# Kernel tuning notes

Hardware: AMD Instinct MI355X
Metric: run time of the kernel (lower is better)

## Reference

```python
import jax, jax.numpy as jnp
import numpy as np

QUERY_DIM, FEAT_DIM, HID_DIM, OUT_DIM = 512, 2048, 512, 512
B, L, S, T = 8, 128, 100, 100


def setup_inputs() -> dict:
    key = jax.random.key(0)
    ks = jax.random.split(key, 9)
    d = {
        "query": jax.random.normal(ks[0], (B, L, QUERY_DIM), jnp.float32),
        "src": jax.random.normal(ks[1], (B, S, FEAT_DIM), jnp.float32),
        "trg": jax.random.normal(ks[2], (B, T, FEAT_DIM), jnp.float32),
        # params (LinearAct == Linear + identity act); src/trg projections share weights
        "Wq": jax.random.normal(ks[3], (QUERY_DIM, HID_DIM), jnp.float32) / np.sqrt(QUERY_DIM),
        "bq": jnp.zeros((HID_DIM,), jnp.float32),
        "Ws": jax.random.normal(ks[4], (FEAT_DIM, HID_DIM), jnp.float32) / np.sqrt(FEAT_DIM),
        "bs": jnp.zeros((HID_DIM,), jnp.float32),
        "Wo": jax.random.normal(ks[5], (HID_DIM + QUERY_DIM, OUT_DIM), jnp.float32) / np.sqrt(HID_DIM + QUERY_DIM),
        "bo": jnp.zeros((OUT_DIM,), jnp.float32),
    }
    return d


def reference(query, src, trg, Wq, bq, Ws, bs, Wo, bo):
    b, l, _ = query.shape
    s = src.shape[1]
    t = trg.shape[1]
    q = query @ Wq + bq          # b,l,k
    s_key = src @ Ws + bs        # b,s,k
    t_key = trg @ Ws + bs        # b,t,k
    hid = q.shape[-1]
    # score[b,l,s,t] = q . (s_key - t_key)/sqrt(2) / sqrt(hid) -- decomposed, no b,s,t,k tensor
    qs = jnp.einsum('blk,bsk->bls', q, s_key)
    qt = jnp.einsum('blk,btk->blt', q, t_key)
    score = (qs[:, :, :, None] - qt[:, :, None, :]) / jnp.sqrt(jnp.asarray(2.0 * hid, q.dtype))
    w = jax.nn.softmax(score.reshape(b, l, s * t), axis=-1).reshape(b, l, s, t)
    # ctx = sum_{s,t} w * (s_key - t_key)/sqrt(2), decomposed via marginals
    ws = w.sum(axis=3)           # b,l,s
    wt = w.sum(axis=2)           # b,l,t
    ctx = (jnp.einsum('bls,bsk->blk', ws, s_key) - jnp.einsum('blt,btk->blk', wt, t_key)) / jnp.sqrt(jnp.asarray(2.0, q.dtype))
    x = jnp.concatenate([query, ctx], axis=-1) @ Wo + bo
    return x
```

## Files before the change

### kernel.cpp

```cpp
#include <hip/hip_runtime.h>
#include <math.h>


typedef __attribute__((ext_vector_type(8))) short s16x8;
typedef __attribute__((ext_vector_type(4))) float f32x4;

__device__ __forceinline__ unsigned short f2bf(float f) {
    unsigned int u = __float_as_uint(f);
    return (unsigned short)((u + 0x7fffu + ((u >> 16) & 1u)) >> 16);
}

__device__ __forceinline__ s16x8 cvt8(const float* p) {
    float4 u = *(const float4*)p, w = *(const float4*)(p + 4);
    s16x8 o;
    o[0] = (short)f2bf(u.x); o[1] = (short)f2bf(u.y);
    o[2] = (short)f2bf(u.z); o[3] = (short)f2bf(u.w);
    o[4] = (short)f2bf(w.x); o[5] = (short)f2bf(w.y);
    o[6] = (short)f2bf(w.z); o[7] = (short)f2bf(w.w);
    return o;
}

__device__ __forceinline__ void gemm64_keys(
    const float* __restrict__ src, const float* __restrict__ trg,
    const float* __restrict__ Ws, unsigned short* __restrict__ Kb,
    int m0, int n0, unsigned short* As, unsigned short* Bs) {
    const int t = threadIdx.x;
    const int lane = t & 63, wid = t >> 6;
    const int wm = (wid & 1) * 32, wn = (wid >> 1) * 32;
    const int lr = lane & 15, lq = lane >> 4;
    const int r = t >> 3, c8 = (t & 7) * 8;
    const int nrow = t >> 2, kc16 = (t & 3) * 16;

    const int ra_row = m0 + r, rb_row = m0 + r + 32;
    const float* arp = (ra_row < 800) ? (src + (size_t)ra_row * 2048)
                                      : (trg + (size_t)(ra_row - 800) * 2048);
    const float* brp = (rb_row < 800) ? (src + (size_t)rb_row * 2048)
                                      : (trg + (size_t)(rb_row - 800) * 2048);

    s16x8 ra0, ra1;
    float bw[16];
#define LDK(kt)                                                              \
    ra0 = cvt8(arp + (kt) + c8);                                             \
    ra1 = cvt8(brp + (kt) + c8);                                             \
    _Pragma("unroll")                                                        \
    for (int j = 0; j < 16; j++)                                             \
        bw[j] = Ws[(size_t)((kt) + kc16 + j) * 512 + n0 + nrow];

    f32x4 acc[2][2] = {};
    LDK(0);
    for (int it = 0; it < 32; it++) {
        __syncthreads();
        *(s16x8*)&As[r * 72 + c8]        = ra0;
        *(s16x8*)&As[(r + 32) * 72 + c8] = ra1;
        {
            s16x8 bb0, bb1;
#pragma unroll
            for (int j = 0; j < 8; j++) {
                bb0[j] = (short)f2bf(bw[j]);
                bb1[j] = (short)f2bf(bw[8 + j]);
            }
            *(s16x8*)&Bs[nrow * 72 + kc16]     = bb0;
            *(s16x8*)&Bs[nrow * 72 + kc16 + 8] = bb1;
        }
        __syncthreads();
        if (it < 31) { LDK((it + 1) * 64); }
#pragma unroll
        for (int s = 0; s < 2; s++) {
            s16x8 a0 = *(const s16x8*)&As[(wm + lr) * 72      + s * 32 + lq * 8];
            s16x8 a1 = *(const s16x8*)&As[(wm + 16 + lr) * 72 + s * 32 + lq * 8];
            s16x8 b0 = *(const s16x8*)&Bs[(wn + lr) * 72      + s * 32 + lq * 8];
            s16x8 b1 = *(const s16x8*)&Bs[(wn + 16 + lr) * 72 + s * 32 + lq * 8];
            acc[0][0] = __builtin_amdgcn_mfma_f32_16x16x32_bf16(a0, b0, acc[0][0], 0, 0, 0);
            acc[0][1] = __builtin_amdgcn_mfma_f32_16x16x32_bf16(a0, b1, acc[0][1], 0, 0, 0);
            acc[1][0] = __builtin_amdgcn_mfma_f32_16x16x32_bf16(a1, b0, acc[1][0], 0, 0, 0);
            acc[1][1] = __builtin_amdgcn_mfma_f32_16x16x32_bf16(a1, b1, acc[1][1], 0, 0, 0);
        }
    }
#undef LDK
#pragma unroll
    for (int i = 0; i < 2; i++)
#pragma unroll
        for (int j = 0; j < 2; j++) {
            const int col = n0 + wn + j * 16 + lr;
            const int row = m0 + wm + i * 16 + lq * 4;
#pragma unroll
            for (int rr = 0; rr < 4; rr++)
                Kb[(size_t)(row + rr) * 512 + col] = f2bf(acc[i][j][rr]);
        }
}

__device__ __forceinline__ void gemm32_rawB(
    const float* __restrict__ A, const float* __restrict__ W,
    const float* __restrict__ bias, unsigned short* __restrict__ C,
    int m0, int n0, unsigned short* As, unsigned short* Bs) {
    const int t = threadIdx.x;
    const int lane = t & 63, wid = t >> 6;
    const int wm = (wid & 1) * 16, wn = (wid >> 1) * 32;
    const int lr = lane & 15, lq = lane >> 4;
    const int r = t >> 3, c8 = (t & 7) * 8;
    const int nrow = t >> 2, kc16 = (t & 3) * 16;

    s16x8 ra;
    float bw[16];
#define LDQ(kt)                                                              \
    ra = cvt8(A + (size_t)(m0 + r) * 512 + (kt) + c8);                       \
    _Pragma("unroll")                                                        \
    for (int j = 0; j < 16; j++)                                             \
        bw[j] = W[(size_t)((kt) + kc16 + j) * 512 + n0 + nrow];

    f32x4 acc[2] = {};
    LDQ(0);
    for (int it = 0; it < 8; it++) {
        __syncthreads();
        *(s16x8*)&As[r * 72 + c8] = ra;
        {
            s16x8 bb0, bb1;
#pragma unroll
            for (int j = 0; j < 8; j++) {
                bb0[j] = (short)f2bf(bw[j]);
                bb1[j] = (short)f2bf(bw[8 + j]);
            }
            *(s16x8*)&Bs[nrow * 72 + kc16]     = bb0;
            *(s16x8*)&Bs[nrow * 72 + kc16 + 8] = bb1;
        }
        __syncthreads();
        if (it < 7) { LDQ((it + 1) * 64); }
#pragma unroll
        for (int s = 0; s < 2; s++) {
            s16x8 a0 = *(const s16x8*)&As[(wm + lr) * 72      + s * 32 + lq * 8];
            s16x8 b0 = *(const s16x8*)&Bs[(wn + lr) * 72      + s * 32 + lq * 8];
            s16x8 b1 = *(const s16x8*)&Bs[(wn + 16 + lr) * 72 + s * 32 + lq * 8];
            acc[0] = __builtin_amdgcn_mfma_f32_16x16x32_bf16(a0, b0, acc[0], 0, 0, 0);
            acc[1] = __builtin_amdgcn_mfma_f32_16x16x32_bf16(a0, b1, acc[1], 0, 0, 0);
        }
    }
#undef LDQ
#pragma unroll
    for (int j = 0; j < 2; j++) {
        const int col = n0 + wn + j * 16 + lr;
        const int row = m0 + wm + lq * 4;
        const float bv = bias[col];
#pragma unroll
        for (int rr = 0; rr < 4; rr++)
            C[(size_t)(row + rr) * 512 + col] = f2bf(acc[j][rr] + bv);
    }
}

__device__ __forceinline__ void gemm32_cvtA(
    const float* __restrict__ A, const unsigned short* __restrict__ BT,
    const float* __restrict__ bias, float* __restrict__ C,
    int m0, int n0, int KB, unsigned short* As, unsigned short* Bs) {
    const int t = threadIdx.x;
    const int lane = t & 63, wid = t >> 6;
    const int wm = (wid & 1) * 16, wn = (wid >> 1) * 32;
    const int lr = lane & 15, lq = lane >> 4;
    const int r = t >> 3, c8 = (t & 7) * 8;

    s16x8 ra, rb0, rb1;
#define LD32(kt)                                                            \
    ra  = cvt8(A + (size_t)(m0 + r) * 512 + (kt) + c8);                     \
    rb0 = *(const s16x8*)(BT + (size_t)(n0 + r)      * KB + (kt) + c8);     \
    rb1 = *(const s16x8*)(BT + (size_t)(n0 + r + 32) * KB + (kt) + c8);

    f32x4 acc[2] = {};
    LD32(0);
    for (int it = 0; it < 8; it++) {
        __syncthreads();
        *(s16x8*)&As[r * 72 + c8]        = ra;
        *(s16x8*)&Bs[r * 72 + c8]        = rb0;
        *(s16x8*)&Bs[(r + 32) * 72 + c8] = rb1;
        __syncthreads();
        if (it < 7) { LD32((it + 1) * 64); }
#pragma unroll
        for (int s = 0; s < 2; s++) {
            s16x8 a0 = *(const s16x8*)&As[(wm + lr) * 72      + s * 32 + lq * 8];
            s16x8 b0 = *(const s16x8*)&Bs[(wn + lr) * 72      + s * 32 + lq * 8];
            s16x8 b1 = *(const s16x8*)&Bs[(wn + 16 + lr) * 72 + s * 32 + lq * 8];
            acc[0] = __builtin_amdgcn_mfma_f32_16x16x32_bf16(a0, b0, acc[0], 0, 0, 0);
            acc[1] = __builtin_amdgcn_mfma_f32_16x16x32_bf16(a0, b1, acc[1], 0, 0, 0);
        }
    }
#undef LD32
#pragma unroll
    for (int j = 0; j < 2; j++) {
        const int col = n0 + wn + j * 16 + lr;
        const int row = m0 + wm + lq * 4;
        const float bv = bias[col];
#pragma unroll
        for (int rr = 0; rr < 4; rr++)
            C[(size_t)(row + rr) * 512 + col] = acc[j][rr] + bv;
    }
}

__device__ __forceinline__ void gemm64_P(
    const unsigned short* __restrict__ Kb, const unsigned short* __restrict__ wotBot,
    float* __restrict__ P, int m0, int n0, unsigned short* As,
    unsigned short* Bs) {
    const int t = threadIdx.x;
    const int lane = t & 63, wid = t >> 6;
    const int wm = (wid & 1) * 32, wn = (wid >> 1) * 32;
    const int lr = lane & 15, lq = lane >> 4;
    const int r = t >> 3, c8 = (t & 7) * 8;

    s16x8 ra0, ra1, rb0, rb1;
#define LDP(kt)                                                               \
    ra0 = *(const s16x8*)(Kb + (size_t)(m0 + r)      * 512 + (kt) + c8);      \
    ra1 = *(const s16x8*)(Kb + (size_t)(m0 + r + 32) * 512 + (kt) + c8);      \
    rb0 = *(const s16x8*)(wotBot + (size_t)(n0 + r)      * 1024 + (kt) + c8); \
    rb1 = *(const s16x8*)(wotBot + (size_t)(n0 + r + 32) * 1024 + (kt) + c8);

    f32x4 acc[2][2] = {};
    LDP(0);
    for (int it = 0; it < 8; it++) {
        __syncthreads();
        *(s16x8*)&As[r * 72 + c8]        = ra0;
        *(s16x8*)&As[(r + 32) * 72 + c8] = ra1;
        *(s16x8*)&Bs[r * 72 + c8]        = rb0;
        *(s16x8*)&Bs[(r + 32) * 72 + c8] = rb1;
        __syncthreads();
        if (it < 7) { LDP((it + 1) * 64); }
#pragma unroll
        for (int s = 0; s < 2; s++) {
            s16x8 a0 = *(const s16x8*)&As[(wm + lr) * 72      + s * 32 + lq * 8];
            s16x8 a1 = *(const s16x8*)&As[(wm + 16 + lr) * 72 + s * 32 + lq * 8];
            s16x8 b0 = *(const s16x8*)&Bs[(wn + lr) * 72      + s * 32 + lq * 8];
            s16x8 b1 = *(const s16x8*)&Bs[(wn + 16 + lr) * 72 + s * 32 + lq * 8];
            acc[0][0] = __builtin_amdgcn_mfma_f32_16x16x32_bf16(a0, b0, acc[0][0], 0, 0, 0);
            acc[0][1] = __builtin_amdgcn_mfma_f32_16x16x32_bf16(a0, b1, acc[0][1], 0, 0, 0);
            acc[1][0] = __builtin_amdgcn_mfma_f32_16x16x32_bf16(a1, b0, acc[1][0], 0, 0, 0);
            acc[1][1] = __builtin_amdgcn_mfma_f32_16x16x32_bf16(a1, b1, acc[1][1], 0, 0, 0);
        }
    }
#undef LDP
#pragma unroll
    for (int i = 0; i < 2; i++)
#pragma unroll
        for (int j = 0; j < 2; j++) {
            const int col = n0 + wn + j * 16 + lr;
            const int row = m0 + wm + i * 16 + lq * 4;
#pragma unroll
            for (int rr = 0; rr < 4; rr++)
                P[(size_t)(row + rr) * 512 + col] = acc[i][j][rr];
        }
}

__global__ __launch_bounds__(256) void k_stage1(
    const float* __restrict__ query, const float* __restrict__ src,
    const float* __restrict__ trg, const float* __restrict__ Wq,
    const float* __restrict__ Ws, const float* __restrict__ Wo,
    const float* __restrict__ bq, unsigned short* __restrict__ qh,
    unsigned short* __restrict__ keysbf, unsigned short* __restrict__ wot) {
    __shared__ __align__(16) unsigned short As[64 * 72];
    __shared__ __align__(16) unsigned short Bs[64 * 72];
    const int bid = blockIdx.x, t = threadIdx.x;

    if (bid < 200) {
        gemm64_keys(src, trg, Ws, keysbf, (bid >> 3) * 64, (bid & 7) * 64,
                    As, Bs);
    } else if (bid < 456) {
        const int rr = bid - 200;
        gemm32_rawB(query, Wq, bq, qh, (rr >> 3) * 32, (rr & 7) * 64, As, Bs);
    } else {
        float (*tile)[33] = (float(*)[33])As;
        const int id2 = bid - 456;
        const int tk = id2 >> 4, tn = id2 & 15;
        const int row = t >> 3, c4 = (t & 7) * 4;
        float4 v = *(const float4*)(Wo + (size_t)(tk * 32 + row) * 512 + tn * 32 + c4);
        tile[row][c4 + 0] = v.x; tile[row][c4 + 1] = v.y;
        tile[row][c4 + 2] = v.z; tile[row][c4 + 3] = v.w;
        __syncthreads();
        ushort4 o = make_ushort4(f2bf(tile[c4 + 0][row]), f2bf(tile[c4 + 1][row]),
                                 f2bf(tile[c4 + 2][row]), f2bf(tile[c4 + 3][row]));
        *(ushort4*)(wot + (size_t)(tn * 32 + row) * 1024 + tk * 32 + c4) = o;
    }
}

__global__ __launch_bounds__(256) void k_stage2(
    const float* __restrict__ query, const unsigned short* __restrict__ qh,
    const unsigned short* __restrict__ keysbf,
    const unsigned short* __restrict__ wot, const float* __restrict__ bo,
    float* __restrict__ sc, float* __restrict__ P, float* __restrict__ out) {
    __shared__ __align__(16) unsigned short As[64 * 72];
    __shared__ __align__(16) unsigned short Bs[64 * 72];
    const int bid = blockIdx.x;
    const int t = threadIdx.x;

    if (bid >= 328) {
        const int rr = bid - 328;
        gemm32_cvtA(query, wot, bo, out, (rr >> 3) * 32, (rr & 7) * 64, 1024,
                    As, Bs);
        return;
    }
    if (bid >= 128) {
        const int rem = bid - 128;
        gemm64_P(keysbf, wot + 512, P, (rem >> 3) * 64, (rem & 7) * 64, As, Bs);
        return;
    }

    const int mt = bid >> 2, nt = bid & 3;
    const int m0 = mt * 32, b = mt >> 2, n0 = nt * 64;
    const int lane = t & 63, wid = t >> 6;
    const int wm = (wid & 1) * 16, wn = (wid >> 1) * 32;
    const int lr = lane & 15, lq = lane >> 4;
    const int r = t >> 3, c8 = (t & 7) * 8;

    const int nA = n0 + r, nB = n0 + r + 32;
    int kr0 = (nA < 128) ? (b * 100 + nA) : (800 + b * 100 + (nA - 128));
    int kr1 = (nB < 128) ? (b * 100 + nB) : (800 + b * 100 + (nB - 128));
    kr0 = kr0 > 1599 ? 1599 : kr0;
    kr1 = kr1 > 1599 ? 1599 : kr1;

    s16x8 ra, rb0, rb1;
#define LDSC(kt)                                                        \
    ra  = *(const s16x8*)(qh + (size_t)(m0 + r) * 512 + (kt) + c8);     \
    rb0 = *(const s16x8*)(keysbf + (size_t)kr0 * 512 + (kt) + c8);      \
    rb1 = *(const s16x8*)(keysbf + (size_t)kr1 * 512 + (kt) + c8);

    f32x4 acc[2] = {};
    LDSC(0);
    for (int it = 0; it < 8; it++) {
        __syncthreads();
        *(s16x8*)&As[r * 72 + c8]        = ra;
        *(s16x8*)&Bs[r * 72 + c8]        = rb0;
        *(s16x8*)&Bs[(r + 32) * 72 + c8] = rb1;
        __syncthreads();
        if (it < 7) { LDSC((it + 1) * 64); }
#pragma unroll
        for (int s = 0; s < 2; s++) {
            s16x8 a0 = *(const s16x8*)&As[(wm + lr) * 72      + s * 32 + lq * 8];
            s16x8 b0 = *(const s16x8*)&Bs[(wn + lr) * 72      + s * 32 + lq * 8];
            s16x8 b1 = *(const s16x8*)&Bs[(wn + 16 + lr) * 72 + s * 32 + lq * 8];
            acc[0] = __builtin_amdgcn_mfma_f32_16x16x32_bf16(a0, b0, acc[0], 0, 0, 0);
            acc[1] = __builtin_amdgcn_mfma_f32_16x16x32_bf16(a0, b1, acc[1], 0, 0, 0);
        }
    }
#undef LDSC
#pragma unroll
    for (int j = 0; j < 2; j++) {
        const int col = n0 + wn + j * 16 + lr;
        const int row = m0 + wm + lq * 4;
        const float scale = (col >= 128) ? -(1.0f / 32.0f) : (1.0f / 32.0f);
#pragma unroll
        for (int rr = 0; rr < 4; rr++)
            sc[(size_t)(row + rr) * 256 + col] = acc[j][rr] * scale;
    }
}

__global__ __launch_bounds__(256) void k_stageD(
    const float* __restrict__ sc, const float* __restrict__ P,
    float* __restrict__ out) {
    __shared__ float wbuf[200 * 33];
    __shared__ float Bs[40 * 32];

    const int t = threadIdx.x;
    const int b = blockIdx.y;
    const int n0 = blockIdx.x * 32;
    const int l0 = blockIdx.z * 32;
    const int wave = t >> 6, lane = t & 63;

    for (int i = 0; i < 8; i++) {
        const int li = wave * 8 + i;
        const float4 v = *(const float4*)(
            sc + (size_t)(b * 128 + l0 + li) * 256 + lane * 4);
        const float vv[4] = {v.x, v.y, v.z, v.w};
        const int c0 = lane * 4;
        float mS = -1e30f, mT = -1e30f;
#pragma unroll
        for (int j = 0; j < 4; j++) {
            const int col = c0 + j;
            if (col < 100) mS = fmaxf(mS, vv[j]);
            if (col >= 128 && col < 228) mT = fmaxf(mT, vv[j]);
        }
#pragma unroll
        for (int off = 32; off > 0; off >>= 1) {
            mS = fmaxf(mS, __shfl_xor(mS, off));
            mT = fmaxf(mT, __shfl_xor(mT, off));
        }
        float eS[4], eT[4], sS = 0.f, sT = 0.f;
#pragma unroll
        for (int j = 0; j < 4; j++) {
            const int col = c0 + j;
            eS[j] = (col < 100) ? __expf(vv[j] - mS) : 0.f;
            eT[j] = (col >= 128 && col < 228) ? __expf(vv[j] - mT) : 0.f;
            sS += eS[j]; sT += eT[j];
        }
#pragma unroll
        for (int off = 32; off > 0; off >>= 1) {
            sS += __shfl_xor(sS, off);
            sT += __shfl_xor(sT, off);
        }
        const float iS = 1.f / sS, iT = 1.f / sT;
#pragma unroll
        for (int j = 0; j < 4; j++) {
            const int col = c0 + j;
            if (col < 100) wbuf[col * 33 + li] = eS[j] * iS;
            if (col >= 128 && col < 228)
                wbuf[(100 + col - 128) * 33 + li] = eT[j] * iT;
        }
    }
    __syncthreads();

    const int tx = t & 7, ty = t >> 3;
    float rB[5];
    auto loadB = [&](int kbase) {
#pragma unroll
        for (int e = 0; e < 5; e++) {
            const int idx = t + e * 256;
            const int k = idx >> 5, j = idx & 31;
            const int kk = kbase + k;
            rB[e] = (kk < 100)
                ?  P[(size_t)(b * 100 + kk) * 512 + n0 + j]
                : -P[(size_t)(800 + b * 100 + (kk - 100)) * 512 + n0 + j];
        }
    };

    float acc[4] = {};
    loadB(0);
    for (int c5 = 0; c5 < 5; c5++) {
        __syncthreads();
#pragma unroll
        for (int e = 0; e < 5; e++) {
            const int idx = t + e * 256;
            Bs[idx] = rB[e];
        }
        __syncthreads();
        if (c5 < 4) loadB((c5 + 1) * 40);
#pragma unroll 8
        for (int k = 0; k < 40; k++) {
            const float ar = wbuf[(c5 * 40 + k) * 33 + ty];
            float br[4];
            *(float4*)br = *(const float4*)&Bs[k * 32 + tx * 4];
#pragma unroll
            for (int j = 0; j < 4; j++) acc[j] = fmaf(ar, br[j], acc[j]);
        }
    }

    const float s2 = 0.70710678118654752f;
    const int m = b * 128 + l0 + ty;
#pragma unroll
    for (int j = 0; j < 4; j++)
        unsafeAtomicAdd(&out[(size_t)m * 512 + n0 + tx * 4 + j], acc[j] * s2);
}


extern "C" void kernel_launch(void* const* d_in, const int* in_sizes, int n_in,
                              void* d_out, int out_size, void* d_ws, size_t ws_size,
                              hipStream_t stream) {
    const float* query = (const float*)d_in[0];
    const float* src   = (const float*)d_in[1];
    const float* trg   = (const float*)d_in[2];
    const float* Wq    = (const float*)d_in[3];
    const float* bq    = (const float*)d_in[4];
    const float* Ws    = (const float*)d_in[5];
    const float* Wo    = (const float*)d_in[7];
    const float* bo    = (const float*)d_in[8];
    float* out = (float*)d_out;

    unsigned short* keysbf = (unsigned short*)d_ws;
    float* sc = (float*)(keysbf + 819200);
    float* P  = sc + 262144;
    unsigned short* qh  = (unsigned short*)(P + 819200);
    unsigned short* wot = qh + 524288;

    k_stage1<<<968, 256, 0, stream>>>(query, src, trg, Wq, Ws, Wo, bq,
                                      qh, keysbf, wot);
    k_stage2<<<584, 256, 0, stream>>>(query, qh, keysbf, wot, bo, sc, P, out);
    k_stageD<<<dim3(16, 8, 4), 256, 0, stream>>>(sc, P, out);
}
```

Baseline: 153.4 us.

## Split-K the key projection GEMM four ways with atomic fp32 accumulation

The src/trg key projection (1600x2048 by 2048x512) is split along K into four chunks of 512, giving 800 blocks instead of 200. Partial sums are accumulated with atomic adds into an fp32 keys buffer that is zeroed by a memset beforehand. Downstream consumers now read fp32 keys and convert them to bf16 on load. This is meant to fill the GPU better during stage 1, at the cost of an extra memset, atomic traffic, and doubled key read bandwidth in stage 2.

```diff
diff --git a/kernel.cpp b/kernel.cpp
--- a/kernel.cpp
+++ b/kernel.cpp
@@ -22,8 +22,8 @@
 
 __device__ __forceinline__ void gemm64_keys(
     const float* __restrict__ src, const float* __restrict__ trg,
-    const float* __restrict__ Ws, unsigned short* __restrict__ Kb,
-    int m0, int n0, unsigned short* As, unsigned short* Bs) {
+    const float* __restrict__ Ws, float* __restrict__ Kf,
+    int m0, int n0, int kbase, unsigned short* As, unsigned short* Bs) {
     const int t = threadIdx.x;
     const int lane = t & 63, wid = t >> 6;
     const int wm = (wid & 1) * 32, wn = (wid >> 1) * 32;
@@ -47,8 +47,8 @@
         bw[j] = Ws[(size_t)((kt) + kc16 + j) * 512 + n0 + nrow];
 
     f32x4 acc[2][2] = {};
-    LDK(0);
-    for (int it = 0; it < 32; it++) {
+    LDK(kbase);
+    for (int it = 0; it < 8; it++) {
         __syncthreads();
         *(s16x8*)&As[r * 72 + c8]        = ra0;
         *(s16x8*)&As[(r + 32) * 72 + c8] = ra1;
@@ -63,7 +63,7 @@
             *(s16x8*)&Bs[nrow * 72 + kc16 + 8] = bb1;
         }
         __syncthreads();
-        if (it < 31) { LDK((it + 1) * 64); }
+        if (it < 7) { LDK(kbase + (it + 1) * 64); }
 #pragma unroll
         for (int s = 0; s < 2; s++) {
             s16x8 a0 = *(const s16x8*)&As[(wm + lr) * 72      + s * 32 + lq * 8];
@@ -85,7 +85,8 @@
             const int row = m0 + wm + i * 16 + lq * 4;
 #pragma unroll
             for (int rr = 0; rr < 4; rr++)
-                Kb[(size_t)(row + rr) * 512 + col] = f2bf(acc[i][j][rr]);
+                unsafeAtomicAdd(&Kf[(size_t)(row + rr) * 512 + col],
+                                acc[i][j][rr]);
         }
 }
 
@@ -193,7 +194,7 @@
 }
 
 __device__ __forceinline__ void gemm64_P(
-    const unsigned short* __restrict__ Kb, const unsigned short* __restrict__ wotBot,
+    const float* __restrict__ Kf, const unsigned short* __restrict__ wotBot,
     float* __restrict__ P, int m0, int n0, unsigned short* As,
     unsigned short* Bs) {
     const int t = threadIdx.x;
@@ -204,8 +205,8 @@
 
     s16x8 ra0, ra1, rb0, rb1;
 #define LDP(kt)                                                               \
-    ra0 = *(const s16x8*)(Kb + (size_t)(m0 + r)      * 512 + (kt) + c8);      \
-    ra1 = *(const s16x8*)(Kb + (size_t)(m0 + r + 32) * 512 + (kt) + c8);      \
+    ra0 = cvt8(Kf + (size_t)(m0 + r)      * 512 + (kt) + c8);                 \
+    ra1 = cvt8(Kf + (size_t)(m0 + r + 32) * 512 + (kt) + c8);                 \
     rb0 = *(const s16x8*)(wotBot + (size_t)(n0 + r)      * 1024 + (kt) + c8); \
     rb1 = *(const s16x8*)(wotBot + (size_t)(n0 + r + 32) * 1024 + (kt) + c8);
 
@@ -249,20 +250,21 @@
     const float* __restrict__ trg, const float* __restrict__ Wq,
     const float* __restrict__ Ws, const float* __restrict__ Wo,
     const float* __restrict__ bq, unsigned short* __restrict__ qh,
-    unsigned short* __restrict__ keysbf, unsigned short* __restrict__ wot) {
+    float* __restrict__ keys, unsigned short* __restrict__ wot) {
     __shared__ __align__(16) unsigned short As[64 * 72];
     __shared__ __align__(16) unsigned short Bs[64 * 72];
     const int bid = blockIdx.x, t = threadIdx.x;
 
-    if (bid < 200) {
-        gemm64_keys(src, trg, Ws, keysbf, (bid >> 3) * 64, (bid & 7) * 64,
-                    As, Bs);
-    } else if (bid < 456) {
-        const int rr = bid - 200;
+    if (bid < 800) {
+        const int c = bid / 200, rem = bid % 200;
+        gemm64_keys(src, trg, Ws, keys, (rem >> 3) * 64, (rem & 7) * 64,
+                    c * 512, As, Bs);
+    } else if (bid < 1056) {
+        const int rr = bid - 800;
         gemm32_rawB(query, Wq, bq, qh, (rr >> 3) * 32, (rr & 7) * 64, As, Bs);
     } else {
         float (*tile)[33] = (float(*)[33])As;
-        const int id2 = bid - 456;
+        const int id2 = bid - 1056;
         const int tk = id2 >> 4, tn = id2 & 15;
         const int row = t >> 3, c4 = (t & 7) * 4;
         float4 v = *(const float4*)(Wo + (size_t)(tk * 32 + row) * 512 + tn * 32 + c4);
@@ -277,9 +279,9 @@
 
 __global__ __launch_bounds__(256) void k_stage2(
     const float* __restrict__ query, const unsigned short* __restrict__ qh,
-    const unsigned short* __restrict__ keysbf,
-    const unsigned short* __restrict__ wot, const float* __restrict__ bo,
-    float* __restrict__ sc, float* __restrict__ P, float* __restrict__ out) {
+    const float* __restrict__ keys, const unsigned short* __restrict__ wot,
+    const float* __restrict__ bo, float* __restrict__ sc,
+    float* __restrict__ P, float* __restrict__ out) {
     __shared__ __align__(16) unsigned short As[64 * 72];
     __shared__ __align__(16) unsigned short Bs[64 * 72];
     const int bid = blockIdx.x;
@@ -293,7 +295,7 @@
     }
     if (bid >= 128) {
         const int rem = bid - 128;
-        gemm64_P(keysbf, wot + 512, P, (rem >> 3) * 64, (rem & 7) * 64, As, Bs);
+        gemm64_P(keys, wot + 512, P, (rem >> 3) * 64, (rem & 7) * 64, As, Bs);
         return;
     }
 
@@ -313,8 +315,8 @@
     s16x8 ra, rb0, rb1;
 #define LDSC(kt)                                                        \
     ra  = *(const s16x8*)(qh + (size_t)(m0 + r) * 512 + (kt) + c8);     \
-    rb0 = *(const s16x8*)(keysbf + (size_t)kr0 * 512 + (kt) + c8);      \
-    rb1 = *(const s16x8*)(keysbf + (size_t)kr1 * 512 + (kt) + c8);
+    rb0 = cvt8(keys + (size_t)kr0 * 512 + (kt) + c8);                   \
+    rb1 = cvt8(keys + (size_t)kr1 * 512 + (kt) + c8);
 
     f32x4 acc[2] = {};
     LDSC(0);
@@ -456,14 +458,15 @@
     const float* bo    = (const float*)d_in[8];
     float* out = (float*)d_out;
 
-    unsigned short* keysbf = (unsigned short*)d_ws;
-    float* sc = (float*)(keysbf + 819200);
-    float* P  = sc + 262144;
+    float* keys = (float*)d_ws;
+    float* sc   = keys + 819200;
+    float* P    = sc + 262144;
     unsigned short* qh  = (unsigned short*)(P + 819200);
     unsigned short* wot = qh + 524288;
 
-    k_stage1<<<968, 256, 0, stream>>>(query, src, trg, Wq, Ws, Wo, bq,
-                                      qh, keysbf, wot);
-    k_stage2<<<584, 256, 0, stream>>>(query, qh, keysbf, wot, bo, sc, P, out);
+    hipMemsetAsync(keys, 0, 1600 * 512 * sizeof(float), stream);
+    k_stage1<<<1568, 256, 0, stream>>>(query, src, trg, Wq, Ws, Wo, bq,
+                                       qh, keys, wot);
+    k_stage2<<<584, 256, 0, stream>>>(query, qh, keys, wot, bo, sc, P, out);
     k_stageD<<<dim3(16, 8, 4), 256, 0, stream>>>(sc, P, out);
 }
```

Result: faster. 142.5 us (-7.1%).
